# Optimization experiments

Measured on AMD Instinct MI355X. Metric: run time of the kernel, lower is better.

Reference implementation:

```python
import jax, jax.numpy as jnp
import numpy as np

NUM_HEADS = 16

def setup_inputs() -> dict:
    key = jax.random.key(0)
    ks = jax.random.split(key, 5)
    b, c, w, h = 2, 1024, 48, 48
    sc = 0.02
    return {
        "x": jax.random.normal(ks[0], (b, c, w, h), jnp.float32),
        "Wqkv": jax.random.normal(ks[1], (3 * c, c), jnp.float32) * sc,
        "bqkv": jax.random.normal(ks[2], (3 * c,), jnp.float32) * sc,
        "Wo": jax.random.normal(ks[3], (c, c), jnp.float32) * sc,
        "bo": jax.random.normal(ks[4], (c,), jnp.float32) * sc,
    }

def reference(x, Wqkv, bqkv, Wo, bo):
    b, c, w, h = x.shape
    n = NUM_HEADS
    hd = c // n
    s = w * h
    # [b,c,w,h] -> tokens [b, s, c]
    xs = x.transpose(0, 2, 3, 1).reshape(b, s, c)
    qkv = xs @ Wqkv.T + bqkv                       # [b, s, 3c]
    # rearrange 'b s (three n hd) -> three b n s hd'
    qkv = qkv.reshape(b, s, 3, n, hd).transpose(2, 0, 3, 1, 4)
    q, k, v = qkv[0], qkv[1], qkv[2]               # [b, n, s, hd]
    score = jnp.einsum('bnqh,bnkh->bnqk', q, k) / jnp.sqrt(jnp.float32(hd))
    # module uses a soft causal mask: subtract 10000 above the diagonal
    mask = 10000.0 * jnp.triu(jnp.ones((s, s), dtype=score.dtype), k=1)
    attn = jax.nn.softmax(score - mask, axis=-1)   # [b, n, s, s]
    z = jnp.einsum('bnqk,bnkh->bqnh', attn, v).reshape(b, s, c)
    out = z @ Wo.T + bo                            # [b, s, c]
    return out.reshape(b, w, h, c).transpose(0, 3, 1, 2)
```

## Files before the change

kernel.cpp:

```cpp
#include <hip/hip_runtime.h>

typedef __bf16 bf16;
typedef __bf16 bf16x8 __attribute__((ext_vector_type(8)));
typedef float floatx4 __attribute__((ext_vector_type(4)));

static constexpr int S = 2304;
static constexpr int C = 1024;
static constexpr int NHEAD = 16;
static constexpr int HDIM = 64;
static constexpr int BATCH = 2;
static constexpr float QSCALE = 0.18033688011112042f;

__global__ __launch_bounds__(256) void k_convert(const float* __restrict__ src,
                                                 bf16* __restrict__ dst, int n8) {
  int i = blockIdx.x * 256 + threadIdx.x;
  if (i >= n8) return;
  float4 a = *(const float4*)(src + (size_t)i * 8);
  float4 b = *(const float4*)(src + (size_t)i * 8 + 4);
  bf16x8 o;
  o[0] = (bf16)a.x; o[1] = (bf16)a.y; o[2] = (bf16)a.z; o[3] = (bf16)a.w;
  o[4] = (bf16)b.x; o[5] = (bf16)b.y; o[6] = (bf16)b.z; o[7] = (bf16)b.w;
  *(bf16x8*)(dst + (size_t)i * 8) = o;
}

__global__ __launch_bounds__(256) void k_transpose(const float* __restrict__ x,
                                                   bf16* __restrict__ xs) {
  __shared__ bf16 T[64 * 72];
  int c0 = blockIdx.x * 64, t0 = blockIdx.y * 64, b = blockIdx.z;
  int tid = threadIdx.x;
  const float* xb = x + (size_t)b * C * S;
#pragma unroll
  for (int it = 0; it < 4; ++it) {
    int idx = it * 256 + tid;
    int rc = idx >> 4, t4 = idx & 15;
    float4 v = *(const float4*)(xb + (size_t)(c0 + rc) * S + t0 + t4 * 4);
    T[(t4 * 4 + 0) * 72 + rc] = (bf16)v.x;
    T[(t4 * 4 + 1) * 72 + rc] = (bf16)v.y;
    T[(t4 * 4 + 2) * 72 + rc] = (bf16)v.z;
    T[(t4 * 4 + 3) * 72 + rc] = (bf16)v.w;
  }
  __syncthreads();
  bf16* xsb = xs + (size_t)b * S * C;
#pragma unroll
  for (int it = 0; it < 2; ++it) {
    int idx = it * 256 + tid;
    int rt = idx >> 3, c8 = idx & 7;
    bf16x8 v;
#pragma unroll
    for (int i = 0; i < 8; ++i) v[i] = T[rt * 72 + c8 * 8 + i];
    *(bf16x8*)(xsb + (size_t)(t0 + rt) * C + c0 + c8 * 8) = v;
  }
}

__device__ __forceinline__ void g2l16(const bf16* g, bf16* l) {
  __builtin_amdgcn_global_load_lds(
      (const __attribute__((address_space(1))) void*)g,
      (__attribute__((address_space(3))) void*)l, 16, 0, 0);
}

template <int EPI>
__global__ __launch_bounds__(256) void k_gemm_bt(const bf16* __restrict__ A,
                                                 const bf16* __restrict__ Bt,
                                                 const float* __restrict__ bias,
                                                 bf16* __restrict__ q,
                                                 bf16* __restrict__ k,
                                                 bf16* __restrict__ v,
                                                 float* __restrict__ outf) {
  constexpr int K = C;
  __shared__ bf16 As[128 * 32];
  __shared__ bf16 Bs[128 * 32];
  int tid = threadIdx.x;
  int w = tid >> 6, lane = tid & 63, ln = lane & 15, quad = lane >> 4;
  int m0 = blockIdx.y * 128, n0 = blockIdx.x * 128;
  int moff = (w >> 1) * 64, noff = (w & 1) * 64;
  floatx4 acc[4][4] = {};

  for (int k0 = 0; k0 < K; k0 += 32) {
    __syncthreads();
#pragma unroll
    for (int it = 0; it < 2; ++it) {
      int cb = (it * 4 + w) * 64;
      int g = cb + lane;
      int row = g >> 2, c4 = g & 3;
      g2l16(A + (size_t)(m0 + row) * K + k0 + c4 * 8, As + cb * 8);
      g2l16(Bt + (size_t)(n0 + row) * K + k0 + c4 * 8, Bs + cb * 8);
    }
    __syncthreads();
    bf16x8 af[4], bfr[4];
#pragma unroll
    for (int i = 0; i < 4; ++i) {
      af[i]  = *(const bf16x8*)(As + (moff + i * 16 + ln) * 32 + quad * 8);
      bfr[i] = *(const bf16x8*)(Bs + (noff + i * 16 + ln) * 32 + quad * 8);
    }
#pragma unroll
    for (int im = 0; im < 4; ++im)
#pragma unroll
      for (int in = 0; in < 4; ++in)
        acc[im][in] = __builtin_amdgcn_mfma_f32_16x16x32_bf16(
            af[im], bfr[in], acc[im][in], 0, 0, 0);
  }

  int bidx = (m0 >= S) ? 1 : 0;
  if (EPI == 0) {
#pragma unroll
    for (int in = 0; in < 4; ++in) {
      int j = n0 + noff + in * 16 + ln;
      float bv = bias[j];
      int three = j >> 10;
      int head = (j >> 6) & 15;
      int hdi = j & 63;
#pragma unroll
      for (int im = 0; im < 4; ++im) {
        int mbase = m0 + moff + im * 16 + quad * 4;
        int tb = mbase - bidx * S;
        if (three == 2) {
          union { ushort4 u; bf16 h[4]; } P;
#pragma unroll
          for (int r = 0; r < 4; ++r) P.h[r] = (bf16)(acc[im][in][r] + bv);
          *(ushort4*)(v + ((size_t)(bidx * NHEAD + head) * HDIM + hdi) * S + tb) = P.u;
        } else if (three == 0) {
          bf16* dst = q + ((size_t)(bidx * NHEAD + head) * S + tb) * HDIM + hdi;
#pragma unroll
          for (int r = 0; r < 4; ++r)
            dst[(size_t)r * HDIM] = (bf16)((acc[im][in][r] + bv) * QSCALE);
        } else {
          bf16* dst = k + ((size_t)(bidx * NHEAD + head) * S + tb) * HDIM + hdi;
#pragma unroll
          for (int r = 0; r < 4; ++r) dst[(size_t)r * HDIM] = (bf16)(acc[im][in][r] + bv);
        }
      }
    }
  } else {
#pragma unroll
    for (int in = 0; in < 4; ++in) {
      int co = n0 + noff + in * 16 + ln;
      float bv = bias[co];
#pragma unroll
      for (int im = 0; im < 4; ++im) {
        int mbase = m0 + moff + im * 16 + quad * 4;
        int tb = mbase - bidx * S;
        float4 st;
        st.x = acc[im][in][0] + bv;
        st.y = acc[im][in][1] + bv;
        st.z = acc[im][in][2] + bv;
        st.w = acc[im][in][3] + bv;
        *(float4*)(outf + ((size_t)bidx * C + co) * S + tb) = st;
      }
    }
  }
}

__global__ __launch_bounds__(256) void k_attn(const bf16* __restrict__ Qg,
                                              const bf16* __restrict__ Kg,
                                              const bf16* __restrict__ Vtg,
                                              bf16* __restrict__ z) {
  __shared__ bf16 Ks[2][64 * 64];
  __shared__ bf16 Vs[2][64 * 64];
  __shared__ bf16 Pt[64 * 64];
  int i = blockIdx.x;
  int xcd = i & 7, j = i >> 3;
  int grp = j / 36, jq = j % 36;
  int qi = 35 - jq;
  int bh = xcd + 8 * grp;
  int b = bh >> 4, h = bh & 15;
  int tid = threadIdx.x;
  int w = tid >> 6, lane = tid & 63, ln = lane & 15, quad = lane >> 4;
  int q0 = qi * 64;
  int qg = q0 + w * 16 + ln;

  const bf16* kb = Kg + (size_t)bh * S * HDIM;
  const bf16* vb = Vtg + (size_t)bh * HDIM * S;

  int s_row = tid >> 3, s_c8 = tid & 7;
  int s_cs = s_c8 ^ (s_row & 7);
  int s_row2 = s_row + 32;
  int s_cs2 = s_c8 ^ (s_row2 & 7);
  size_t kOff1 = (size_t)s_row * HDIM + s_cs * 8;
  size_t kOff2 = (size_t)s_row2 * HDIM + s_cs2 * 8;
  size_t vOff1 = (size_t)s_row * S + s_cs * 8;
  size_t vOff2 = (size_t)s_row2 * S + s_cs2 * 8;

  const bf16* qb = Qg + ((size_t)bh * S + qg) * HDIM + quad * 8;
  bf16x8 qf0 = *(const bf16x8*)qb;
  bf16x8 qf1 = *(const bf16x8*)(qb + 32);

  float lsum = 0.f;
  floatx4 o_acc[4] = {};

  int prow = w * 16 + ln;
  int psw = ln & 7;
  bf16* ptw = Pt + prow * 64 + (quad & 1) * 4;
  const bf16* ptr = Pt + prow * 64;

  g2l16(kb + kOff1, Ks[0] + tid * 8);
  g2l16(vb + vOff1, Vs[0] + tid * 8);
  g2l16(kb + kOff2, Ks[0] + (256 + tid) * 8);
  g2l16(vb + vOff2, Vs[0] + (256 + tid) * 8);

  const bf16* kbn = kb + (size_t)64 * HDIM;
  const bf16* vbn = vb + 64;

#pragma unroll 1
  for (int kt = 0; kt <= qi; ++kt) {
    int cur = kt & 1;
    __syncthreads();

    if (kt < qi) {
      bf16* kd = Ks[1 - cur];
      bf16* vd = Vs[1 - cur];
      g2l16(kbn + kOff1, kd + tid * 8);
      g2l16(vbn + vOff1, vd + tid * 8);
      g2l16(kbn + kOff2, kd + (256 + tid) * 8);
      g2l16(vbn + vOff2, vd + (256 + tid) * 8);
      kbn += (size_t)64 * HDIM;
      vbn += 64;
    }

    floatx4 s_acc[4] = {};
#pragma unroll
    for (int kf = 0; kf < 4; ++kf) {
      int row = kf * 16 + ln;
      int sw = row & 7;
      bf16x8 k0 = *(const bf16x8*)(Ks[cur] + row * 64 + (sw ^ quad) * 8);
      bf16x8 k1 = *(const bf16x8*)(Ks[cur] + row * 64 + ((4 ^ sw) ^ quad) * 8);
      s_acc[kf] = __builtin_amdgcn_mfma_f32_16x16x32_bf16(k0, qf0, s_acc[kf], 0, 0, 0);
      s_acc[kf] = __builtin_amdgcn_mfma_f32_16x16x32_bf16(k1, qf1, s_acc[kf], 0, 0, 0);
    }

    if (kt < qi) {
#pragma unroll
      for (int kf = 0; kf < 4; ++kf) {
        union { ushort4 u; bf16 hh[4]; } P;
#pragma unroll
        for (int r = 0; r < 4; ++r) {
          float pv = exp2f(s_acc[kf][r]);
          lsum += pv;
          P.hh[r] = (bf16)pv;
        }
        *(ushort4*)(ptw + (((kf * 2 + (quad >> 1)) ^ psw)) * 8) = P.u;
      }
    } else {
#pragma unroll
      for (int kf = 0; kf < 4; ++kf) {
        union { ushort4 u; bf16 hh[4]; } P;
#pragma unroll
        for (int r = 0; r < 4; ++r) {
          int kl = kf * 16 + quad * 4 + r;
          float pv = (kl > w * 16 + ln) ? 0.f : exp2f(s_acc[kf][r]);
          lsum += pv;
          P.hh[r] = (bf16)pv;
        }
        *(ushort4*)(ptw + (((kf * 2 + (quad >> 1)) ^ psw)) * 8) = P.u;
      }
    }

#pragma unroll
    for (int t = 0; t < 2; ++t) {
      bf16x8 pf = *(const bf16x8*)(ptr + (((t * 4 + quad) ^ psw)) * 8);
#pragma unroll
      for (int hf = 0; hf < 4; ++hf) {
        int row = hf * 16 + ln;
        int sw = row & 7;
        bf16x8 vf = *(const bf16x8*)(Vs[cur] + row * 64 + (((t * 4 + quad) ^ sw)) * 8);
        o_acc[hf] = __builtin_amdgcn_mfma_f32_16x16x32_bf16(vf, pf, o_acc[hf], 0, 0, 0);
      }
    }
  }

  lsum += __shfl_xor(lsum, 16);
  lsum += __shfl_xor(lsum, 32);
  float inv = 1.f / lsum;

  bf16* dst = z + ((size_t)b * S + qg) * C + h * HDIM + quad * 4;
#pragma unroll
  for (int hf = 0; hf < 4; ++hf) {
    union { ushort4 u; bf16 hh[4]; } P;
#pragma unroll
    for (int r = 0; r < 4; ++r) P.hh[r] = (bf16)(o_acc[hf][r] * inv);
    *(ushort4*)(dst + hf * 16) = P.u;
  }
}

extern "C" void kernel_launch(void* const* d_in, const int* in_sizes, int n_in,
                              void* d_out, int out_size, void* d_ws, size_t ws_size,
                              hipStream_t stream) {
  const float* x    = (const float*)d_in[0];
  const float* Wqkv = (const float*)d_in[1];
  const float* bqkv = (const float*)d_in[2];
  const float* Wo   = (const float*)d_in[3];
  const float* bo   = (const float*)d_in[4];
  float* out = (float*)d_out;

  bf16* ws = (bf16*)d_ws;
  const size_t tok = (size_t)BATCH * S * C;
  bf16* xs   = ws;
  bf16* Qg   = ws + tok;
  bf16* Kg   = ws + 2 * tok;
  bf16* Vtg  = ws + 3 * tok;
  bf16* Wqb  = ws + 4 * tok;
  bf16* Wob  = Wqb + (size_t)3 * C * C;
  bf16* z    = xs;

  k_convert<<<(3 * C * C / 8 + 255) / 256, 256, 0, stream>>>(Wqkv, Wqb, 3 * C * C / 8);
  k_convert<<<(C * C / 8 + 255) / 256, 256, 0, stream>>>(Wo, Wob, C * C / 8);
  k_transpose<<<dim3(C / 64, S / 64, BATCH), 256, 0, stream>>>(x, xs);
  k_gemm_bt<0><<<dim3(3 * C / 128, BATCH * S / 128), 256, 0, stream>>>(
      xs, Wqb, bqkv, Qg, Kg, Vtg, nullptr);
  k_attn<<<dim3(1152), 256, 0, stream>>>(Qg, Kg, Vtg, z);
  k_gemm_bt<1><<<dim3(C / 128, BATCH * S / 128), 256, 0, stream>>>(
      z, Wob, bo, nullptr, nullptr, nullptr, out);
}
```

Before: 227.7 us.

## Split long causal attention rows across two blocks with atomic accumulation

Query tiles with index 18 and above now have their key range split between two blocks. Each block adds its unnormalized output and its row sum into fp32 global buffers with atomicAdd, and a new normalize kernel then divides and writes bf16 z. Shorter query tiles still run in a single block. This cuts the longest per-block work from 36 key tiles to 18, which should improve load balance and the tail of the attention grid. The price is a zeroing kernel, a large volume of fp32 atomics, an extra kernel launch and a round trip through the fp32 buffers.

```diff
diff --git a/kernel.cpp b/kernel.cpp
--- a/kernel.cpp
+++ b/kernel.cpp
@@ -10,6 +10,13 @@
 static constexpr int HDIM = 64;
 static constexpr int BATCH = 2;
 static constexpr float QSCALE = 0.18033688011112042f;
+static constexpr int QSPLIT = 18;
+static constexpr int NACC = S - QSPLIT * 64;
+
+__global__ __launch_bounds__(256) void k_zero(float4* __restrict__ p, int n4) {
+  int i = blockIdx.x * 256 + threadIdx.x;
+  if (i < n4) p[i] = float4{0.f, 0.f, 0.f, 0.f};
+}
 
 __global__ __launch_bounds__(256) void k_convert(const float* __restrict__ src,
                                                  bf16* __restrict__ dst, int n8) {
@@ -150,18 +157,31 @@
   }
 }
 
-__global__ __launch_bounds__(256) void k_attn(const bf16* __restrict__ Qg,
-                                              const bf16* __restrict__ Kg,
-                                              const bf16* __restrict__ Vtg,
-                                              bf16* __restrict__ z) {
+__global__ __launch_bounds__(256) void k_attn_part(const bf16* __restrict__ Qg,
+                                                   const bf16* __restrict__ Kg,
+                                                   const bf16* __restrict__ Vtg,
+                                                   bf16* __restrict__ z,
+                                                   float* __restrict__ Oacc,
+                                                   float* __restrict__ Lacc) {
   __shared__ bf16 Ks[2][64 * 64];
   __shared__ bf16 Vs[2][64 * 64];
   __shared__ bf16 Pt[64 * 64];
   int i = blockIdx.x;
   int xcd = i & 7, j = i >> 3;
-  int grp = j / 36, jq = j % 36;
-  int qi = 35 - jq;
+  int grp = j / 54, r = j % 54;
   int bh = xcd + 8 * grp;
+  int qi, lo, hi;
+  bool single = (r >= 36);
+  if (!single) {
+    qi = 35 - (r >> 1);
+    int c = r & 1;
+    lo = c * (qi + 1) / 2;
+    hi = (c + 1) * (qi + 1) / 2;
+  } else {
+    qi = 53 - r;
+    lo = 0;
+    hi = qi + 1;
+  }
   int b = bh >> 4, h = bh & 15;
   int tid = threadIdx.x;
   int w = tid >> 6, lane = tid & 63, ln = lane & 15, quad = lane >> 4;
@@ -192,20 +212,22 @@
   bf16* ptw = Pt + prow * 64 + (quad & 1) * 4;
   const bf16* ptr = Pt + prow * 64;
 
-  g2l16(kb + kOff1, Ks[0] + tid * 8);
-  g2l16(vb + vOff1, Vs[0] + tid * 8);
-  g2l16(kb + kOff2, Ks[0] + (256 + tid) * 8);
-  g2l16(vb + vOff2, Vs[0] + (256 + tid) * 8);
-
-  const bf16* kbn = kb + (size_t)64 * HDIM;
-  const bf16* vbn = vb + 64;
+  const bf16* kb0 = kb + (size_t)lo * 64 * HDIM;
+  const bf16* vb0 = vb + (size_t)lo * 64;
+  g2l16(kb0 + kOff1, Ks[0] + tid * 8);
+  g2l16(vb0 + vOff1, Vs[0] + tid * 8);
+  g2l16(kb0 + kOff2, Ks[0] + (256 + tid) * 8);
+  g2l16(vb0 + vOff2, Vs[0] + (256 + tid) * 8);
+
+  const bf16* kbn = kb0 + (size_t)64 * HDIM;
+  const bf16* vbn = vb0 + 64;
 
 #pragma unroll 1
-  for (int kt = 0; kt <= qi; ++kt) {
-    int cur = kt & 1;
+  for (int kt = lo; kt < hi; ++kt) {
+    int cur = (kt - lo) & 1;
     __syncthreads();
 
-    if (kt < qi) {
+    if (kt + 1 < hi) {
       bf16* kd = Ks[1 - cur];
       bf16* vd = Vs[1 - cur];
       g2l16(kbn + kOff1, kd + tid * 8);
@@ -232,10 +254,10 @@
       for (int kf = 0; kf < 4; ++kf) {
         union { ushort4 u; bf16 hh[4]; } P;
 #pragma unroll
-        for (int r = 0; r < 4; ++r) {
-          float pv = exp2f(s_acc[kf][r]);
+        for (int rr = 0; rr < 4; ++rr) {
+          float pv = exp2f(s_acc[kf][rr]);
           lsum += pv;
-          P.hh[r] = (bf16)pv;
+          P.hh[rr] = (bf16)pv;
         }
         *(ushort4*)(ptw + (((kf * 2 + (quad >> 1)) ^ psw)) * 8) = P.u;
       }
@@ -244,11 +266,11 @@
       for (int kf = 0; kf < 4; ++kf) {
         union { ushort4 u; bf16 hh[4]; } P;
 #pragma unroll
-        for (int r = 0; r < 4; ++r) {
-          int kl = kf * 16 + quad * 4 + r;
-          float pv = (kl > w * 16 + ln) ? 0.f : exp2f(s_acc[kf][r]);
+        for (int rr = 0; rr < 4; ++rr) {
+          int kl = kf * 16 + quad * 4 + rr;
+          float pv = (kl > w * 16 + ln) ? 0.f : exp2f(s_acc[kf][rr]);
           lsum += pv;
-          P.hh[r] = (bf16)pv;
+          P.hh[rr] = (bf16)pv;
         }
         *(ushort4*)(ptw + (((kf * 2 + (quad >> 1)) ^ psw)) * 8) = P.u;
       }
@@ -269,15 +291,59 @@
 
   lsum += __shfl_xor(lsum, 16);
   lsum += __shfl_xor(lsum, 32);
-  float inv = 1.f / lsum;
-
-  bf16* dst = z + ((size_t)b * S + qg) * C + h * HDIM + quad * 4;
+
+  if (single) {
+    float inv = 1.f / lsum;
+    bf16* dst = z + ((size_t)b * S + qg) * C + h * HDIM + quad * 4;
+#pragma unroll
+    for (int hf = 0; hf < 4; ++hf) {
+      union { ushort4 u; bf16 hh[4]; } P;
+#pragma unroll
+      for (int rr = 0; rr < 4; ++rr) P.hh[rr] = (bf16)(o_acc[hf][rr] * inv);
+      *(ushort4*)(dst + hf * 16) = P.u;
+    }
+  } else {
+    int qa = qg - QSPLIT * 64;
+    if (lane < 16) atomicAdd(&Lacc[bh * NACC + qa], lsum);
+#pragma unroll
+    for (int hf = 0; hf < 4; ++hf)
+#pragma unroll
+      for (int rr = 0; rr < 4; ++rr)
+        atomicAdd(&Oacc[((size_t)bh * 64 + hf * 16 + quad * 4 + rr) * NACC + qa],
+                  o_acc[hf][rr]);
+  }
+}
+
+__global__ __launch_bounds__(256) void k_norm(const float* __restrict__ Oacc,
+                                              const float* __restrict__ Lacc,
+                                              bf16* __restrict__ z) {
+  __shared__ float T[64 * 65];
+  int qt = blockIdx.x, bh = blockIdx.y;
+  int b = bh >> 4, h = bh & 15;
+  int qrel0 = qt * 64;
+  int q0 = QSPLIT * 64 + qrel0;
+  int tid = threadIdx.x;
+  int q4 = (tid & 15) * 4, hd0 = tid >> 4;
+  float4 lv = *(const float4*)(Lacc + bh * NACC + qrel0 + q4);
+  float inv0 = 1.f / lv.x, inv1 = 1.f / lv.y, inv2 = 1.f / lv.z, inv3 = 1.f / lv.w;
 #pragma unroll
   for (int hf = 0; hf < 4; ++hf) {
-    union { ushort4 u; bf16 hh[4]; } P;
-#pragma unroll
-    for (int r = 0; r < 4; ++r) P.hh[r] = (bf16)(o_acc[hf][r] * inv);
-    *(ushort4*)(dst + hf * 16) = P.u;
+    int hd = hf * 16 + hd0;
+    float4 v = *(const float4*)(Oacc + ((size_t)bh * 64 + hd) * NACC + qrel0 + q4);
+    T[(q4 + 0) * 65 + hd] = v.x * inv0;
+    T[(q4 + 1) * 65 + hd] = v.y * inv1;
+    T[(q4 + 2) * 65 + hd] = v.z * inv2;
+    T[(q4 + 3) * 65 + hd] = v.w * inv3;
+  }
+  __syncthreads();
+#pragma unroll
+  for (int it = 0; it < 2; ++it) {
+    int idx = it * 256 + tid;
+    int qq = idx >> 3, c8 = idx & 7;
+    bf16x8 o;
+#pragma unroll
+    for (int k = 0; k < 8; ++k) o[k] = (bf16)T[qq * 65 + c8 * 8 + k];
+    *(bf16x8*)(z + ((size_t)b * S + q0 + qq) * C + h * HDIM + c8 * 8) = o;
   }
 }
 
@@ -299,14 +365,18 @@
   bf16* Vtg  = ws + 3 * tok;
   bf16* Wqb  = ws + 4 * tok;
   bf16* Wob  = Wqb + (size_t)3 * C * C;
+  float* Oacc = (float*)(Wob + (size_t)C * C);
+  float* Lacc = Oacc + (size_t)32 * 64 * NACC;
   bf16* z    = xs;
 
+  k_zero<<<2340, 256, 0, stream>>>((float4*)Oacc, 599040);
   k_convert<<<(3 * C * C / 8 + 255) / 256, 256, 0, stream>>>(Wqkv, Wqb, 3 * C * C / 8);
   k_convert<<<(C * C / 8 + 255) / 256, 256, 0, stream>>>(Wo, Wob, C * C / 8);
   k_transpose<<<dim3(C / 64, S / 64, BATCH), 256, 0, stream>>>(x, xs);
   k_gemm_bt<0><<<dim3(3 * C / 128, BATCH * S / 128), 256, 0, stream>>>(
       xs, Wqb, bqkv, Qg, Kg, Vtg, nullptr);
-  k_attn<<<dim3(1152), 256, 0, stream>>>(Qg, Kg, Vtg, z);
+  k_attn_part<<<dim3(1728), 256, 0, stream>>>(Qg, Kg, Vtg, z, Oacc, Lacc);
+  k_norm<<<dim3(18, 32), 256, 0, stream>>>(Oacc, Lacc, z);
   k_gemm_bt<1><<<dim3(C / 128, BATCH * S / 128), 256, 0, stream>>>(
       z, Wob, bo, nullptr, nullptr, nullptr, out);
 }
```

Result: no change. 224.3 us (-1.5%).
